# Kernel tuning notes

Hardware: AMD Instinct MI355X
Metric: run time of the kernel (lower is better)

Reference implementation:

```python
import jax, jax.numpy as jnp
import numpy as np
import math

D_MODEL = 512
D_K = 64
B, S = 8, 2048
NEG_INF = -1.0e9


def setup_inputs() -> dict:
    key = jax.random.key(0)
    ks = jax.random.split(key, 10)
    inp = {
        "query_source": jax.random.normal(ks[0], (B, S, D_MODEL), dtype=jnp.float32),
        "key_source": jax.random.normal(ks[1], (B, S, D_MODEL), dtype=jnp.float32),
        "value_source": jax.random.normal(ks[2], (B, S, D_MODEL), dtype=jnp.float32),
        # causal mask: 1 means "masked" (future positions), matching masked_fill(mask == 1, -1e9)
        "mask": jnp.triu(jnp.ones((S, S), dtype=jnp.int32), k=1),
        # Linear weights stored as [in, out] so x @ W + b matches torch Linear
        "Wq": jax.random.normal(ks[3], (D_MODEL, D_K), dtype=jnp.float32) / math.sqrt(D_MODEL),
        "bq": jax.random.normal(ks[4], (D_K,), dtype=jnp.float32) * 0.01,
        "Wk": jax.random.normal(ks[5], (D_MODEL, D_K), dtype=jnp.float32) / math.sqrt(D_MODEL),
        "bk": jax.random.normal(ks[6], (D_K,), dtype=jnp.float32) * 0.01,
        "Wv": jax.random.normal(ks[7], (D_MODEL, D_K), dtype=jnp.float32) / math.sqrt(D_MODEL),
        "bv": jax.random.normal(ks[8], (D_K,), dtype=jnp.float32) * 0.01,
    }
    return inp


def reference(query_source, key_source, value_source, mask, Wq, bq, Wk, bk, Wv, bv):
    d_k = Wq.shape[-1]
    Q = query_source @ Wq + bq          # [B, S, d_k]
    K = key_source @ Wk + bk            # [B, S, d_k]
    V = value_source @ Wv + bv          # [B, S, d_k]
    scores = jnp.einsum("bqd,bkd->bqk", Q, K) / jnp.sqrt(jnp.float32(d_k))  # [B, S, S]
    scores = jnp.where(mask == 1, jnp.float32(NEG_INF), scores)
    attn = jax.nn.softmax(scores, axis=-1)
    return jnp.einsum("bqk,bkd->bqd", attn, V)  # [B, S, d_k]
```

## Files before the change

kernel.cpp:

```cpp
#include <hip/hip_runtime.h>

#define BATCH 8
#define SEQ 2048
#define DMODEL 512
#define DK 64

typedef __attribute__((ext_vector_type(8))) short short8;
typedef __attribute__((ext_vector_type(4))) float f32x4;

__device__ __forceinline__ unsigned f2bfbits(float f) {
  unsigned u = __builtin_bit_cast(unsigned, f);
  return (u + 0x7FFFu + ((u >> 16) & 1u)) >> 16;
}

__device__ __forceinline__ void glds16(const void* g, void* l) {
  __builtin_amdgcn_global_load_lds(
      (const __attribute__((address_space(1))) unsigned int*)g,
      (__attribute__((address_space(3))) unsigned int*)l, 16, 0, 0);
}

#define MFMA_BF16(a, b, c) __builtin_amdgcn_mfma_f32_16x16x32_bf16((a), (b), (c), 0, 0, 0)

__global__ __launch_bounds__(256) void wtrans_kernel(
    const float* __restrict__ Wq, const float* __restrict__ Wk,
    const float* __restrict__ Wv, unsigned short* __restrict__ Wt)
{
  const int p = blockIdx.y;
  const float* W = (p == 0) ? Wq : (p == 1) ? Wk : Wv;
  const int t = threadIdx.x;
  const int c = t & 63;
  const int k0 = blockIdx.x * 64 + (t >> 6) * 16;
  unsigned short* dst = Wt + (p * 64 + c) * 512;
  #pragma unroll
  for (int i = 0; i < 16; ++i) {
    int k = k0 + i;
    dst[k] = (unsigned short)f2bfbits(W[k * 64 + c]);
  }
}

__global__ __launch_bounds__(256) void proj_kernel(
    const float* __restrict__ Xq, const float* __restrict__ Xk, const float* __restrict__ Xv,
    const unsigned short* __restrict__ Wt,
    const float* __restrict__ bq, const float* __restrict__ bk, const float* __restrict__ bv,
    unsigned short* __restrict__ oq, unsigned short* __restrict__ ok,
    unsigned short* __restrict__ ov)
{
  __shared__ __attribute__((aligned(16))) short xs[64 * 128];
  __shared__ __attribute__((aligned(16))) short wt[64 * 128];

  const int p = blockIdx.y;
  const float* X    = (p == 0) ? Xq : (p == 1) ? Xk : Xv;
  const float* bias = (p == 0) ? bq : (p == 1) ? bk : bv;
  unsigned short* out = (p == 0) ? oq : (p == 1) ? ok : ov;
  const float scale = (p == 0) ? 0.125f : 1.0f;
  const unsigned short* Wtp = Wt + p * 64 * 512;

  const int tid = threadIdx.x;
  const long row0 = (long)blockIdx.x * 64;
  const int w = tid >> 6, lane = tid & 63, m = lane & 15, quad = lane >> 4;
  const int xm = m & 7;

  f32x4 acc[4];
  #pragma unroll
  for (int c = 0; c < 4; ++c) acc[c] = (f32x4){0.f, 0.f, 0.f, 0.f};

  for (int h = 0; h < 4; ++h) {
    const int k0 = h * 128;
    if (h) __syncthreads();

    #pragma unroll
    for (int t = 0; t < 4; ++t) {
      int row = w * 16 + t * 4 + (lane >> 4);
      int lc = (lane & 15) ^ (row & 7);
      glds16(Wtp + row * 512 + k0 + lc * 8, &wt[(w * 16 + t * 4) * 128]);
    }

    #pragma unroll
    for (int i = 0; i < 4; ++i) {
      int row = (tid >> 4) + 16 * i;
      int lc = tid & 15;
      const float* xp = X + (row0 + row) * DMODEL + k0 + lc * 8;
      float4 v0 = *(const float4*)xp;
      float4 v1 = *(const float4*)(xp + 4);
      uint4 pk;
      pk.x = f2bfbits(v0.x) | (f2bfbits(v0.y) << 16);
      pk.y = f2bfbits(v0.z) | (f2bfbits(v0.w) << 16);
      pk.z = f2bfbits(v1.x) | (f2bfbits(v1.y) << 16);
      pk.w = f2bfbits(v1.z) | (f2bfbits(v1.w) << 16);
      int pc = lc ^ (row & 7);
      *(uint4*)&xs[row * 128 + pc * 8] = pk;
    }
    __syncthreads();

    #pragma unroll
    for (int s = 0; s < 4; ++s) {
      const int ch0 = ((s * 4 + quad) ^ xm) * 8;
      short8 aF = *(const short8*)&xs[(w * 16 + m) * 128 + ch0];
      #pragma unroll
      for (int c = 0; c < 4; ++c) {
        short8 bF = *(const short8*)&wt[(c * 16 + m) * 128 + ch0];
        acc[c] = MFMA_BF16(aF, bF, acc[c]);
      }
    }
  }

  float bbv[4];
  #pragma unroll
  for (int c = 0; c < 4; ++c) bbv[c] = bias[c * 16 + m];

  if (p < 2) {
    #pragma unroll
    for (int c = 0; c < 4; ++c) {
      #pragma unroll
      for (int r = 0; r < 4; ++r) {
        long row = row0 + w * 16 + quad * 4 + r;
        float v = (acc[c][r] + bbv[c]) * scale;
        out[row * DK + c * 16 + m] = (unsigned short)f2bfbits(v);
      }
    }
  } else {
    long b = row0 >> 11;
    int sbase = (int)(row0 & 2047) + w * 16 + quad * 4;
    #pragma unroll
    for (int c = 0; c < 4; ++c) {
      unsigned lo = f2bfbits(acc[c][0] + bbv[c]) | (f2bfbits(acc[c][1] + bbv[c]) << 16);
      unsigned hi = f2bfbits(acc[c][2] + bbv[c]) | (f2bfbits(acc[c][3] + bbv[c]) << 16);
      *(uint2*)(out + ((long)(b * 64 + c * 16 + m)) * SEQ + sbase) = make_uint2(lo, hi);
    }
  }
}

__global__ __launch_bounds__(256) void attn_kernel(
    const unsigned short* __restrict__ Qb,
    const unsigned short* __restrict__ Kb,
    const unsigned short* __restrict__ Vtg,
    float* __restrict__ out)
{
  __shared__ __attribute__((aligned(16))) short ks[2][64 * 64];
  __shared__ __attribute__((aligned(16))) short vt[2][64 * 64];
  __shared__ __attribute__((aligned(16))) short ps[4][16 * 72];

  const int tid = threadIdx.x;
  const int bi = blockIdx.x & 7;
  const int qt = 31 - (blockIdx.x >> 3);
  const int q0 = qt << 6;
  const int w = tid >> 6, lane = tid & 63, m = lane & 15, quad = lane >> 4;
  const int xm = m & 7;

  const int qrow = q0 + w * 16 + m;
  const unsigned short* qp = Qb + ((long)(bi * SEQ + qrow)) * DK + quad * 8;
  const short8 qA0 = *(const short8*)qp;
  const short8 qA1 = *(const short8*)(qp + 32);

  f32x4 o[4];
  #pragma unroll
  for (int d = 0; d < 4; ++d) o[d] = (f32x4){0.f, 0.f, 0.f, 0.f};
  float psum[4] = {0.f, 0.f, 0.f, 0.f};

  const int nt = qt + 1;

  const int srow = lane >> 3;
  const int slc  = (lane & 7) ^ srow;

  auto stage = [&](int buf, int k0) {
    #pragma unroll
    for (int t = 0; t < 2; ++t) {
      const int row = w * 16 + t * 8 + srow;
      glds16(Kb + ((long)(bi * SEQ + k0 + row)) * DK + slc * 8,
             &ks[buf][(w * 16 + t * 8) * 64]);
      glds16(Vtg + ((long)(bi * DK + row)) * SEQ + k0 + slc * 8,
             &vt[buf][(w * 16 + t * 8) * 64]);
    }
  };

  stage(0, 0);

  for (int kt = 0; kt < nt; ++kt) {
    __syncthreads();
    if (kt + 1 < nt) stage((kt + 1) & 1, (kt + 1) << 6);

    const short* ksb = &ks[kt & 1][0];
    const short* vtb = &vt[kt & 1][0];

    f32x4 sc[4];
    #pragma unroll
    for (int c = 0; c < 4; ++c) {
      const short* kr = ksb + (c * 16 + m) * 64;
      f32x4 a = {0.f, 0.f, 0.f, 0.f};
      a = MFMA_BF16(qA0, *(const short8*)(kr + ((quad ^ xm) * 8)), a);
      a = MFMA_BF16(qA1, *(const short8*)(kr + (((4 + quad) ^ xm) * 8)), a);
      sc[c] = a;
    }

    if (kt == nt - 1) {
      const int rb = q0 + w * 16 + quad * 4;
      const int k0 = kt << 6;
      #pragma unroll
      for (int c = 0; c < 4; ++c) {
        const int col = k0 + c * 16 + m;
        #pragma unroll
        for (int r = 0; r < 4; ++r)
          if (col > rb + r) sc[c][r] = -1e9f;
      }
    }

    #pragma unroll
    for (int c = 0; c < 4; ++c) {
      #pragma unroll
      for (int r = 0; r < 4; ++r)
        sc[c][r] = __expf(sc[c][r]);
    }
    #pragma unroll
    for (int r = 0; r < 4; ++r)
      psum[r] += (sc[0][r] + sc[1][r]) + (sc[2][r] + sc[3][r]);

    short* pw = &ps[w][0];
    #pragma unroll
    for (int c = 0; c < 4; ++c) {
      #pragma unroll
      for (int r = 0; r < 4; ++r)
        pw[(quad * 4 + r) * 72 + c * 16 + m] = (short)f2bfbits(sc[c][r]);
    }
    asm volatile("s_waitcnt lgkmcnt(0)" ::: "memory");

    const short8 pA0 = *(const short8*)(pw + m * 72 + quad * 8);
    const short8 pA1 = *(const short8*)(pw + m * 72 + quad * 8 + 32);

    #pragma unroll
    for (int d = 0; d < 4; ++d) {
      const short* vr = vtb + (d * 16 + m) * 64;
      o[d] = MFMA_BF16(pA0, *(const short8*)(vr + ((quad ^ xm) * 8)), o[d]);
      o[d] = MFMA_BF16(pA1, *(const short8*)(vr + (((4 + quad) ^ xm) * 8)), o[d]);
    }
  }

  #pragma unroll
  for (int off = 1; off < 16; off <<= 1) {
    #pragma unroll
    for (int r = 0; r < 4; ++r)
      psum[r] += __shfl_xor(psum[r], off);
  }

  const int rb = q0 + w * 16 + quad * 4;
  #pragma unroll
  for (int r = 0; r < 4; ++r) {
    const float inv = 1.0f / psum[r];
    float* op = out + ((long)(bi * SEQ + rb + r)) * DK + m;
    op[0]  = o[0][r] * inv;
    op[16] = o[1][r] * inv;
    op[32] = o[2][r] * inv;
    op[48] = o[3][r] * inv;
  }
}

extern "C" void kernel_launch(void* const* d_in, const int* in_sizes, int n_in,
                              void* d_out, int out_size, void* d_ws, size_t ws_size,
                              hipStream_t stream) {
  const float* qs   = (const float*)d_in[0];
  const float* ksrc = (const float*)d_in[1];
  const float* vsrc = (const float*)d_in[2];
  const float* Wq = (const float*)d_in[4];
  const float* bq = (const float*)d_in[5];
  const float* Wk = (const float*)d_in[6];
  const float* bk = (const float*)d_in[7];
  const float* Wv = (const float*)d_in[8];
  const float* bv = (const float*)d_in[9];

  unsigned short* Qb  = (unsigned short*)d_ws;
  unsigned short* Kb  = Qb + (long)BATCH * SEQ * DK;
  unsigned short* Vtg = Kb + (long)BATCH * SEQ * DK;
  unsigned short* Wtg = (unsigned short*)d_out;
  float* outp = (float*)d_out;

  wtrans_kernel<<<dim3(8, 3), dim3(256), 0, stream>>>(Wq, Wk, Wv, Wtg);
  proj_kernel<<<dim3(256, 3), dim3(256), 0, stream>>>(
      qs, ksrc, vsrc, Wtg, bq, bk, bv, Qb, Kb, Vtg);
  attn_kernel<<<dim3(256), dim3(256), 0, stream>>>(Qb, Kb, Vtg, outp);
}
```

Before: 185.3 us.

## Split causal attention across KV chunks and add combine kernel; double-buffer projection

The attention kernel is split so each block handles up to four KV tiles of one query tile. This raises the grid from 256 to 1152 blocks and evens out the work imbalance from the causal triangle. Because softmax here uses no max subtraction, each block writes unnormalized partial outputs and row sums to workspace, and a new combine kernel adds them and normalizes. The projection kernel also gets double-buffered LDS staging so the next K-slice loads overlap with the MFMAs. The cost is extra global traffic for the fp32 partials, plus one more kernel launch.

```diff
diff --git a/kernel.cpp b/kernel.cpp
--- a/kernel.cpp
+++ b/kernel.cpp
@@ -45,8 +45,8 @@
     unsigned short* __restrict__ oq, unsigned short* __restrict__ ok,
     unsigned short* __restrict__ ov)
 {
-  __shared__ __attribute__((aligned(16))) short xs[64 * 128];
-  __shared__ __attribute__((aligned(16))) short wt[64 * 128];
+  __shared__ __attribute__((aligned(16))) short xs[2][64 * 128];
+  __shared__ __attribute__((aligned(16))) short wt[2][64 * 128];
 
   const int p = blockIdx.y;
   const float* X    = (p == 0) ? Xq : (p == 1) ? Xk : Xv;
@@ -64,17 +64,13 @@
   #pragma unroll
   for (int c = 0; c < 4; ++c) acc[c] = (f32x4){0.f, 0.f, 0.f, 0.f};
 
-  for (int h = 0; h < 4; ++h) {
-    const int k0 = h * 128;
-    if (h) __syncthreads();
-
+  auto stage = [&](int buf, int k0) {
     #pragma unroll
     for (int t = 0; t < 4; ++t) {
       int row = w * 16 + t * 4 + (lane >> 4);
       int lc = (lane & 15) ^ (row & 7);
-      glds16(Wtp + row * 512 + k0 + lc * 8, &wt[(w * 16 + t * 4) * 128]);
-    }
-
+      glds16(Wtp + row * 512 + k0 + lc * 8, &wt[buf][(w * 16 + t * 4) * 128]);
+    }
     #pragma unroll
     for (int i = 0; i < 4; ++i) {
       int row = (tid >> 4) + 16 * i;
@@ -88,17 +84,26 @@
       pk.z = f2bfbits(v1.x) | (f2bfbits(v1.y) << 16);
       pk.w = f2bfbits(v1.z) | (f2bfbits(v1.w) << 16);
       int pc = lc ^ (row & 7);
-      *(uint4*)&xs[row * 128 + pc * 8] = pk;
-    }
+      *(uint4*)&xs[buf][row * 128 + pc * 8] = pk;
+    }
+  };
+
+  stage(0, 0);
+
+  #pragma unroll
+  for (int h = 0; h < 4; ++h) {
     __syncthreads();
-
+    if (h < 3) stage((h + 1) & 1, (h + 1) * 128);
+
+    const short* xb = &xs[h & 1][0];
+    const short* wb = &wt[h & 1][0];
     #pragma unroll
     for (int s = 0; s < 4; ++s) {
       const int ch0 = ((s * 4 + quad) ^ xm) * 8;
-      short8 aF = *(const short8*)&xs[(w * 16 + m) * 128 + ch0];
+      short8 aF = *(const short8*)&xb[(w * 16 + m) * 128 + ch0];
       #pragma unroll
       for (int c = 0; c < 4; ++c) {
-        short8 bF = *(const short8*)&wt[(c * 16 + m) * 128 + ch0];
+        short8 bF = *(const short8*)&wb[(c * 16 + m) * 128 + ch0];
         acc[c] = MFMA_BF16(aF, bF, acc[c]);
       }
     }
@@ -134,7 +139,8 @@
     const unsigned short* __restrict__ Qb,
     const unsigned short* __restrict__ Kb,
     const unsigned short* __restrict__ Vtg,
-    float* __restrict__ out)
+    float* __restrict__ Opart,
+    float* __restrict__ lpart)
 {
   __shared__ __attribute__((aligned(16))) short ks[2][64 * 64];
   __shared__ __attribute__((aligned(16))) short vt[2][64 * 64];
@@ -142,8 +148,21 @@
 
   const int tid = threadIdx.x;
   const int bi = blockIdx.x & 7;
-  const int qt = 31 - (blockIdx.x >> 3);
+  const int j = blockIdx.x >> 3;
+
+  int qt = 0, c = 0;
+  {
+    int jj = j;
+    for (qt = 0; qt < 32; ++qt) {
+      int cnt = (qt >> 2) + 1;
+      if (jj < cnt) { c = jj; break; }
+      jj -= cnt;
+    }
+  }
   const int q0 = qt << 6;
+  const int kt0 = c << 2;
+  const int ntc = min(4, qt + 1 - (c << 2));
+
   const int w = tid >> 6, lane = tid & 63, m = lane & 15, quad = lane >> 4;
   const int xm = m & 7;
 
@@ -157,12 +176,11 @@
   for (int d = 0; d < 4; ++d) o[d] = (f32x4){0.f, 0.f, 0.f, 0.f};
   float psum[4] = {0.f, 0.f, 0.f, 0.f};
 
-  const int nt = qt + 1;
-
   const int srow = lane >> 3;
   const int slc  = (lane & 7) ^ srow;
 
-  auto stage = [&](int buf, int k0) {
+  auto stage = [&](int buf, int ktg) {
+    const int k0 = ktg << 6;
     #pragma unroll
     for (int t = 0; t < 2; ++t) {
       const int row = w * 16 + t * 8 + srow;
@@ -173,42 +191,43 @@
     }
   };
 
-  stage(0, 0);
-
-  for (int kt = 0; kt < nt; ++kt) {
+  stage(0, kt0);
+
+  for (int i = 0; i < ntc; ++i) {
     __syncthreads();
-    if (kt + 1 < nt) stage((kt + 1) & 1, (kt + 1) << 6);
-
-    const short* ksb = &ks[kt & 1][0];
-    const short* vtb = &vt[kt & 1][0];
+    if (i + 1 < ntc) stage((i + 1) & 1, kt0 + i + 1);
+
+    const int ktg = kt0 + i;
+    const short* ksb = &ks[i & 1][0];
+    const short* vtb = &vt[i & 1][0];
 
     f32x4 sc[4];
     #pragma unroll
-    for (int c = 0; c < 4; ++c) {
-      const short* kr = ksb + (c * 16 + m) * 64;
+    for (int cc = 0; cc < 4; ++cc) {
+      const short* kr = ksb + (cc * 16 + m) * 64;
       f32x4 a = {0.f, 0.f, 0.f, 0.f};
       a = MFMA_BF16(qA0, *(const short8*)(kr + ((quad ^ xm) * 8)), a);
       a = MFMA_BF16(qA1, *(const short8*)(kr + (((4 + quad) ^ xm) * 8)), a);
-      sc[c] = a;
-    }
-
-    if (kt == nt - 1) {
+      sc[cc] = a;
+    }
+
+    if (ktg == qt) {
       const int rb = q0 + w * 16 + quad * 4;
-      const int k0 = kt << 6;
-      #pragma unroll
-      for (int c = 0; c < 4; ++c) {
-        const int col = k0 + c * 16 + m;
+      const int k0g = ktg << 6;
+      #pragma unroll
+      for (int cc = 0; cc < 4; ++cc) {
+        const int col = k0g + cc * 16 + m;
         #pragma unroll
         for (int r = 0; r < 4; ++r)
-          if (col > rb + r) sc[c][r] = -1e9f;
+          if (col > rb + r) sc[cc][r] = -1e9f;
       }
     }
 
     #pragma unroll
-    for (int c = 0; c < 4; ++c) {
+    for (int cc = 0; cc < 4; ++cc) {
       #pragma unroll
       for (int r = 0; r < 4; ++r)
-        sc[c][r] = __expf(sc[c][r]);
+        sc[cc][r] = __expf(sc[cc][r]);
     }
     #pragma unroll
     for (int r = 0; r < 4; ++r)
@@ -216,10 +235,10 @@
 
     short* pw = &ps[w][0];
     #pragma unroll
-    for (int c = 0; c < 4; ++c) {
+    for (int cc = 0; cc < 4; ++cc) {
       #pragma unroll
       for (int r = 0; r < 4; ++r)
-        pw[(quad * 4 + r) * 72 + c * 16 + m] = (short)f2bfbits(sc[c][r]);
+        pw[(quad * 4 + r) * 72 + cc * 16 + m] = (short)f2bfbits(sc[cc][r]);
     }
     asm volatile("s_waitcnt lgkmcnt(0)" ::: "memory");
 
@@ -241,16 +260,60 @@
       psum[r] += __shfl_xor(psum[r], off);
   }
 
-  const int rb = q0 + w * 16 + quad * 4;
+  const int pi = bi * 144 + j;
+  float* opp = Opart + (long)pi * 4096;
+  const int rb = w * 16 + quad * 4;
   #pragma unroll
   for (int r = 0; r < 4; ++r) {
-    const float inv = 1.0f / psum[r];
-    float* op = out + ((long)(bi * SEQ + rb + r)) * DK + m;
-    op[0]  = o[0][r] * inv;
-    op[16] = o[1][r] * inv;
-    op[32] = o[2][r] * inv;
-    op[48] = o[3][r] * inv;
-  }
+    float* op = opp + (rb + r) * 64 + m;
+    op[0]  = o[0][r];
+    op[16] = o[1][r];
+    op[32] = o[2][r];
+    op[48] = o[3][r];
+  }
+  if (m == 0) {
+    #pragma unroll
+    for (int r = 0; r < 4; ++r)
+      lpart[pi * 64 + rb + r] = psum[r];
+  }
+}
+
+__global__ __launch_bounds__(256) void combine_kernel(
+    const float* __restrict__ Opart, const float* __restrict__ lpart,
+    float* __restrict__ out)
+{
+  const int bi = blockIdx.x & 7;
+  const int qt = blockIdx.x >> 3;
+  const int g = qt >> 2, r = qt & 3;
+  const int base = bi * 144 + (g + 1) * (2 * g + r);
+  const int cnt = g + 1;
+
+  __shared__ float linv[64];
+  const int tid = threadIdx.x;
+  if (tid < 64) {
+    float s = 0.f;
+    for (int i = 0; i < cnt; ++i) s += lpart[(base + i) * 64 + tid];
+    linv[tid] = 1.0f / s;
+  }
+  __syncthreads();
+
+  const int row = tid >> 2;
+  const int col0 = (tid & 3) << 4;
+  f32x4 a0 = {0.f,0.f,0.f,0.f}, a1 = a0, a2 = a0, a3 = a0;
+  for (int i = 0; i < cnt; ++i) {
+    const float4* op = (const float4*)(Opart + (long)(base + i) * 4096 + row * 64 + col0);
+    float4 t0 = op[0], t1 = op[1], t2 = op[2], t3 = op[3];
+    a0[0]+=t0.x; a0[1]+=t0.y; a0[2]+=t0.z; a0[3]+=t0.w;
+    a1[0]+=t1.x; a1[1]+=t1.y; a1[2]+=t1.z; a1[3]+=t1.w;
+    a2[0]+=t2.x; a2[1]+=t2.y; a2[2]+=t2.z; a2[3]+=t2.w;
+    a3[0]+=t3.x; a3[1]+=t3.y; a3[2]+=t3.z; a3[3]+=t3.w;
+  }
+  const float inv = linv[row];
+  float4* dst = (float4*)(out + ((long)(bi * SEQ + (qt << 6) + row)) * DK + col0);
+  dst[0] = make_float4(a0[0]*inv, a0[1]*inv, a0[2]*inv, a0[3]*inv);
+  dst[1] = make_float4(a1[0]*inv, a1[1]*inv, a1[2]*inv, a1[3]*inv);
+  dst[2] = make_float4(a2[0]*inv, a2[1]*inv, a2[2]*inv, a2[3]*inv);
+  dst[3] = make_float4(a3[0]*inv, a3[1]*inv, a3[2]*inv, a3[3]*inv);
 }
 
 extern "C" void kernel_launch(void* const* d_in, const int* in_sizes, int n_in,
@@ -269,11 +332,14 @@
   unsigned short* Qb  = (unsigned short*)d_ws;
   unsigned short* Kb  = Qb + (long)BATCH * SEQ * DK;
   unsigned short* Vtg = Kb + (long)BATCH * SEQ * DK;
+  float* Opart = (float*)(Vtg + (long)BATCH * SEQ * DK);
+  float* lpart = Opart + (long)1152 * 64 * 64;
   unsigned short* Wtg = (unsigned short*)d_out;
   float* outp = (float*)d_out;
 
   wtrans_kernel<<<dim3(8, 3), dim3(256), 0, stream>>>(Wq, Wk, Wv, Wtg);
   proj_kernel<<<dim3(256, 3), dim3(256), 0, stream>>>(
       qs, ksrc, vsrc, Wtg, bq, bk, bv, Qb, Kb, Vtg);
-  attn_kernel<<<dim3(256), dim3(256), 0, stream>>>(Qb, Kb, Vtg, outp);
-}
+  attn_kernel<<<dim3(1152), dim3(256), 0, stream>>>(Qb, Kb, Vtg, Opart, lpart);
+  combine_kernel<<<dim3(256), dim3(256), 0, stream>>>(Opart, lpart, outp);
+}
```

Measured after the change: 178.1 us. -3.9%, faster.
